# Kernel optimization log

Hardware: AMD Instinct MI355X
Metric: run time of the kernel (lower is better)

The kernel has to match this reference:

```python
import jax, jax.numpy as jnp
import numpy as np

B, N, C, H = 16, 4096, 256, 4
D = C // H

def setup_inputs() -> dict:
    key = jax.random.key(0)
    ks = jax.random.split(key, 8)
    w = 0.01  # small init, mimics xavier_uniform gain=0.1
    x = jax.random.normal(ks[0], (B, N, C), jnp.float32)
    S = jax.random.normal(ks[1], (B, H, D, D), jnp.float32) * 0.1
    Wq = jax.random.normal(ks[2], (C, C), jnp.float32) * w
    Wk = jax.random.normal(ks[3], (C, C), jnp.float32) * w
    Wv = jax.random.normal(ks[4], (C, C), jnp.float32) * w
    Wb = jax.random.normal(ks[5], (H, C), jnp.float32) * w  # beta_proj (zeros in torch init; random for nontrivial math)
    Wo = jax.random.normal(ks[6], (C, C), jnp.float32) * w
    g_rms = jnp.ones((C,), jnp.float32)
    return {"x": x, "S": S, "Wq": Wq, "Wk": Wk, "Wv": Wv, "Wb": Wb, "Wo": Wo, "g_rms": g_rms}

def reference(x, S, Wq, Wk, Wv, Wb, Wo, g_rms):
    b, n, c = x.shape
    h = Wb.shape[0]
    d = c // h
    # projections -> (B,H,N,D)
    q = (x @ Wq.T).reshape(b, n, h, d).transpose(0, 2, 1, 3)
    k = (x @ Wk.T).reshape(b, n, h, d).transpose(0, 2, 1, 3)
    v = (x @ Wv.T).reshape(b, n, h, d).transpose(0, 2, 1, 3)
    # feature map + L2 normalize keys
    k = jax.nn.elu(k) + 1.0
    k = k / (jnp.linalg.norm(k, axis=-1, keepdims=True) + 1e-6)
    # per-head gates (B,H,N,1)
    beta = jax.nn.sigmoid(jnp.einsum('bnc,hc->bhn', x, Wb))[..., None]
    # decay + state read
    Sd = S * 0.95
    y = jnp.einsum('bhij,bhnj->bhni', Sd, q)
    pred = jnp.einsum('bhij,bhnj->bhni', Sd, k)
    # delta-rule write: outer(mean weighted error, mean key)
    w_err = jnp.mean(beta * (v - pred), axis=2)  # (B,H,D)
    w_key = jnp.mean(k, axis=2)                  # (B,H,D)
    S_new = jnp.clip(Sd + jnp.einsum('bhi,bhj->bhij', w_err, w_key), -10.0, 10.0)
    # merge heads, RMSNorm, output projection
    y = y.transpose(0, 2, 1, 3).reshape(b, n, c)
    y = y * jax.lax.rsqrt(jnp.mean(y * y, axis=-1, keepdims=True) + 1e-6) * g_rms
    out = y @ Wo.T
    return out, S_new
```

## Files before the change

### kernel.cpp

```cpp
#include <hip/hip_runtime.h>
#include <math.h>


typedef _Float16 f16;
typedef f16 f16x8 __attribute__((ext_vector_type(8)));
typedef float f32x4 __attribute__((ext_vector_type(4)));

__device__ __forceinline__ f16x8 cvt8(const float* q) {
  float4 a = *(const float4*)q;
  float4 b = *(const float4*)(q + 4);
  f16x8 r;
  r[0] = (f16)a.x; r[1] = (f16)a.y; r[2] = (f16)a.z; r[3] = (f16)a.w;
  r[4] = (f16)b.x; r[5] = (f16)b.y; r[6] = (f16)b.z; r[7] = (f16)b.w;
  return r;
}

__global__ __launch_bounds__(256) void beta_xbsum(
    const float* __restrict__ x, const float* __restrict__ Wb,
    float* __restrict__ betaArr, float* __restrict__ xbsum) {
  const int t = threadIdx.x;
  const int wave = t >> 6, lane = t & 63;
  const int b = blockIdx.x >> 6;
  const int tile = blockIdx.x & 63;
  float4 wb[4];
#pragma unroll
  for (int h = 0; h < 4; ++h) wb[h] = *(const float4*)(Wb + h * 256 + lane * 4);
  float xacc[4][4] = {};
  const size_t rowbase = (size_t)b * 4096 + tile * 64;
  __shared__ float bsh[4][64];
  float4 xv = *(const float4*)(x + (rowbase + wave) * 256 + lane * 4);
#pragma unroll 2
  for (int i = 0; i < 16; ++i) {
    int r = i * 4 + wave;
    float4 nx = xv;
    if (i < 15)
      nx = *(const float4*)(x + (rowbase + r + 4) * 256 + lane * 4);
#pragma unroll
    for (int h = 0; h < 4; ++h) {
      float s = xv.x * wb[h].x + xv.y * wb[h].y + xv.z * wb[h].z + xv.w * wb[h].w;
#pragma unroll
      for (int off = 32; off; off >>= 1) s += __shfl_xor(s, off);
      float bh = 1.f / (1.f + __expf(-s));
      if (lane == h) bsh[h][r] = bh;
      xacc[h][0] += bh * xv.x; xacc[h][1] += bh * xv.y;
      xacc[h][2] += bh * xv.z; xacc[h][3] += bh * xv.w;
    }
    xv = nx;
  }
  __shared__ float xbp[4][4][256];
#pragma unroll
  for (int h = 0; h < 4; ++h)
#pragma unroll
    for (int j = 0; j < 4; ++j) xbp[wave][h][lane * 4 + j] = xacc[h][j];
  __syncthreads();
  {
    int h = t >> 6, r = t & 63;
    betaArr[((size_t)(b * 4 + h) << 12) + tile * 64 + r] = bsh[h][r];
  }
  for (int idx = t; idx < 1024; idx += 256) {
    int h = idx >> 8, c = idx & 255;
    float s = xbp[0][h][c] + xbp[1][h][c] + xbp[2][h][c] + xbp[3][h][c];
    atomicAdd(&xbsum[(b * 4 + h) * 256 + c], s);
  }
}

__global__ __launch_bounds__(256) void kgemm_sums(
    const float* __restrict__ x, const float* __restrict__ Wk,
    const float* __restrict__ betaArr,
    float* __restrict__ ksum, float* __restrict__ kbsum) {
  __shared__ union {
    struct { f16 A[128][72]; f16 B[128][72]; } s;
    f16 K[128][132];
  } u;
  __shared__ float bstage[2][128];
  const int t = threadIdx.x;
  const int m0 = blockIdx.y * 128;
  const int n0 = blockIdx.x * 128;
  const int b = m0 >> 12;
  const int wave = t >> 6, lane = t & 63;
  const int wm = (wave >> 1) * 64, wn = (wave & 1) * 64;
  const int fr = lane & 15, fq = lane >> 4;
  {
    int hh = t >> 7, r = t & 127;
    bstage[hh][r] =
        betaArr[((size_t)(b * 4 + (n0 >> 6) + hh) << 12) + (m0 & 4095) + r];
  }
  f32x4 acc[4][4] = {};
#pragma unroll 1
  for (int kt = 0; kt < 4; ++kt) {
    const int k0 = kt * 64;
#pragma unroll
    for (int i = 0; i < 4; ++i) {
      int id = i * 256 + t;
      int row = id >> 3, cc = id & 7;
      *(f16x8*)&u.s.A[row][cc * 8] =
          cvt8(x + (size_t)(m0 + row) * 256 + k0 + cc * 8);
      *(f16x8*)&u.s.B[row][cc * 8] =
          cvt8(Wk + (size_t)(n0 + row) * 256 + k0 + cc * 8);
    }
    __syncthreads();
#pragma unroll
    for (int ks = 0; ks < 2; ++ks) {
      f16x8 afr[4], bfr[4];
#pragma unroll
      for (int mi = 0; mi < 4; ++mi)
        afr[mi] = *(const f16x8*)&u.s.A[wm + mi * 16 + fr][ks * 32 + fq * 8];
#pragma unroll
      for (int ni = 0; ni < 4; ++ni)
        bfr[ni] = *(const f16x8*)&u.s.B[wn + ni * 16 + fr][ks * 32 + fq * 8];
#pragma unroll
      for (int mi = 0; mi < 4; ++mi)
#pragma unroll
        for (int ni = 0; ni < 4; ++ni)
          acc[mi][ni] = __builtin_amdgcn_mfma_f32_16x16x32_f16(
              afr[mi], bfr[ni], acc[mi][ni], 0, 0, 0);
    }
    __syncthreads();
  }
#pragma unroll
  for (int mi = 0; mi < 4; ++mi)
#pragma unroll
    for (int rr = 0; rr < 4; ++rr) {
      float s = 0.f;
#pragma unroll
      for (int ni = 0; ni < 4; ++ni) {
        float v = acc[mi][ni][rr];
        v = v > 0.f ? v + 1.f : __expf(v);
        acc[mi][ni][rr] = v;
        s += v * v;
      }
#pragma unroll
      for (int off = 1; off < 16; off <<= 1) s += __shfl_xor(s, off);
      float inv = 1.f / (sqrtf(s) + 1e-6f);
#pragma unroll
      for (int ni = 0; ni < 4; ++ni) acc[mi][ni][rr] *= inv;
    }
#pragma unroll
  for (int mi = 0; mi < 4; ++mi)
#pragma unroll
    for (int ni = 0; ni < 4; ++ni)
#pragma unroll
      for (int rr = 0; rr < 4; ++rr)
        u.K[wm + mi * 16 + fq * 4 + rr][wn + ni * 16 + fr] = (f16)acc[mi][ni][rr];
  __syncthreads();
  if (t < 128) {
    const int c = t, hl = c >> 6;
    float sk = 0.f, skb = 0.f;
#pragma unroll 4
    for (int r = 0; r < 128; ++r) {
      float v = (float)u.K[r][c];
      float be = bstage[hl][r];
      sk += v;
      skb += be * v;
    }
    int gh = b * 4 + (n0 >> 6) + hl;
    atomicAdd(&ksum[gh * 64 + (c & 63)], sk);
    atomicAdd(&kbsum[gh * 64 + (c & 63)], skb);
  }
}

__global__ __launch_bounds__(256) void fold_M(
    const float* __restrict__ S, const float* __restrict__ Wq,
    f16* __restrict__ M) {
  const int bh = blockIdx.y;
  const int dq = blockIdx.x;
  const int h = bh & 3;
  const int t = threadIdx.x;
  const float* Sp = S + (size_t)bh * 4096 + dq * 8 * 64;
  const float* Wp = Wq + (size_t)h * 64 * 256 + t;
  float m[8] = {};
#pragma unroll 4
  for (int e = 0; e < 64; ++e) {
    float wv = Wp[e * 256];
#pragma unroll
    for (int dd = 0; dd < 8; ++dd) m[dd] += Sp[dd * 64 + e] * wv;
  }
  f16* Mb = M + (size_t)(bh >> 2) * 65536;
#pragma unroll
  for (int dd = 0; dd < 8; ++dd)
    Mb[(size_t)(h * 64 + dq * 8 + dd) * 256 + t] = (f16)(0.95f * m[dd]);
}

__global__ __launch_bounds__(256) void ygemm_ssq(
    const float* __restrict__ x, int m_base, const f16* __restrict__ M,
    f16* __restrict__ y, float* __restrict__ rowssq) {
  __shared__ f16 As[128][72];
  __shared__ f16 Bs[128][72];
  const int t = threadIdx.x;
  const int m0 = blockIdx.y * 128;
  const int n0 = blockIdx.x * 128;
  const int b = (m_base + m0) >> 12;
  const f16* Mb = M + (size_t)b * 65536;
  const int wave = t >> 6, lane = t & 63;
  const int wm = (wave >> 1) * 64, wn = (wave & 1) * 64;
  const int fr = lane & 15, fq = lane >> 4;
  f32x4 acc[4][4] = {};
#pragma unroll 1
  for (int kt = 0; kt < 4; ++kt) {
    const int k0 = kt * 64;
#pragma unroll
    for (int i = 0; i < 4; ++i) {
      int id = i * 256 + t;
      int row = id >> 3, cc = id & 7;
      *(f16x8*)&As[row][cc * 8] =
          cvt8(x + (size_t)(m_base + m0 + row) * 256 + k0 + cc * 8);
      *(uint4*)&Bs[row][cc * 8] =
          *(const uint4*)(Mb + (size_t)(n0 + row) * 256 + k0 + cc * 8);
    }
    __syncthreads();
#pragma unroll
    for (int ks = 0; ks < 2; ++ks) {
      f16x8 afr[4], bfr[4];
#pragma unroll
      for (int mi = 0; mi < 4; ++mi)
        afr[mi] = *(const f16x8*)&As[wm + mi * 16 + fr][ks * 32 + fq * 8];
#pragma unroll
      for (int ni = 0; ni < 4; ++ni)
        bfr[ni] = *(const f16x8*)&Bs[wn + ni * 16 + fr][ks * 32 + fq * 8];
#pragma unroll
      for (int mi = 0; mi < 4; ++mi)
#pragma unroll
        for (int ni = 0; ni < 4; ++ni)
          acc[mi][ni] = __builtin_amdgcn_mfma_f32_16x16x32_f16(
              afr[mi], bfr[ni], acc[mi][ni], 0, 0, 0);
    }
    __syncthreads();
  }
#pragma unroll
  for (int mi = 0; mi < 4; ++mi)
#pragma unroll
    for (int rr = 0; rr < 4; ++rr) {
      float s = 0.f;
#pragma unroll
      for (int ni = 0; ni < 4; ++ni) {
        float v = acc[mi][ni][rr];
        s += v * v;
        int row = m0 + wm + mi * 16 + fq * 4 + rr;
        int col = n0 + wn + ni * 16 + fr;
        y[(size_t)row * 256 + col] = (f16)v;
      }
#pragma unroll
      for (int off = 1; off < 16; off <<= 1) s += __shfl_xor(s, off);
      if (fr == 0)
        atomicAdd(&rowssq[m0 + wm + mi * 16 + fq * 4 + rr], s);
    }
}

__global__ __launch_bounds__(256) void ogemm_scaled(
    const f16* __restrict__ y, const float* __restrict__ rowssq,
    const float* __restrict__ g_rms, const float* __restrict__ Wo,
    float* __restrict__ out, int m_base) {
  __shared__ f16 As[128][72];
  __shared__ f16 Bs[128][72];
  const int t = threadIdx.x;
  const int m0 = blockIdx.y * 128;
  const int n0 = blockIdx.x * 128;
  const int wave = t >> 6, lane = t & 63;
  const int wm = (wave >> 1) * 64, wn = (wave & 1) * 64;
  const int fr = lane & 15, fq = lane >> 4;
  f32x4 acc[4][4] = {};
#pragma unroll 1
  for (int kt = 0; kt < 4; ++kt) {
    const int k0 = kt * 64;
#pragma unroll
    for (int i = 0; i < 4; ++i) {
      int id = i * 256 + t;
      int row = id >> 3, cc = id & 7;
      float rs = rsqrtf(rowssq[m0 + row] * (1.f / 256.f) + 1e-6f);
      const f16* yp = y + (size_t)(m0 + row) * 256 + k0 + cc * 8;
      const float* gp = g_rms + k0 + cc * 8;
      f16x8 a;
#pragma unroll
      for (int j = 0; j < 8; ++j) a[j] = (f16)((float)yp[j] * rs * gp[j]);
      *(f16x8*)&As[row][cc * 8] = a;
      *(f16x8*)&Bs[row][cc * 8] =
          cvt8(Wo + (size_t)(n0 + row) * 256 + k0 + cc * 8);
    }
    __syncthreads();
#pragma unroll
    for (int ks = 0; ks < 2; ++ks) {
      f16x8 afr[4], bfr[4];
#pragma unroll
      for (int mi = 0; mi < 4; ++mi)
        afr[mi] = *(const f16x8*)&As[wm + mi * 16 + fr][ks * 32 + fq * 8];
#pragma unroll
      for (int ni = 0; ni < 4; ++ni)
        bfr[ni] = *(const f16x8*)&Bs[wn + ni * 16 + fr][ks * 32 + fq * 8];
#pragma unroll
      for (int mi = 0; mi < 4; ++mi)
#pragma unroll
        for (int ni = 0; ni < 4; ++ni)
          acc[mi][ni] = __builtin_amdgcn_mfma_f32_16x16x32_f16(
              afr[mi], bfr[ni], acc[mi][ni], 0, 0, 0);
    }
    __syncthreads();
  }
#pragma unroll
  for (int mi = 0; mi < 4; ++mi)
#pragma unroll
    for (int ni = 0; ni < 4; ++ni)
#pragma unroll
      for (int rr = 0; rr < 4; ++rr) {
        int row = m_base + m0 + wm + mi * 16 + fq * 4 + rr;
        int col = n0 + wn + ni * 16 + fr;
        out[(size_t)row * 256 + col] = acc[mi][ni][rr];
      }
}

__global__ __launch_bounds__(256) void finalize_S(
    const float* __restrict__ S, const float* __restrict__ Wv,
    const float* __restrict__ xbsum, const float* __restrict__ ksum,
    const float* __restrict__ kbsum, float* __restrict__ Sout) {
  const int bh = blockIdx.x;
  const int h = bh & 3;
  const int t = threadIdx.x;
  const int wave = t >> 6, lane = t & 63;
  __shared__ float xb[256], kb[64], key[64], errv[64];
  xb[t] = xbsum[bh * 256 + t];
  if (t < 64) {
    kb[t] = kbsum[bh * 64 + t];
    key[t] = ksum[bh * 64 + t] * (1.f / 4096.f);
  }
  __syncthreads();
#pragma unroll 1
  for (int ri = 0; ri < 16; ++ri) {
    int i = wave * 16 + ri;
    float4 wv4 = *(const float4*)(Wv + (size_t)(h * 64 + i) * 256 + lane * 4);
    float4 xb4 = *(const float4*)(&xb[lane * 4]);
    float s = wv4.x * xb4.x + wv4.y * xb4.y + wv4.z * xb4.z + wv4.w * xb4.w;
    s -= 0.95f * S[(size_t)bh * 4096 + i * 64 + lane] * kb[lane];
#pragma unroll
    for (int off = 32; off; off >>= 1) s += __shfl_xor(s, off);
    if (lane == 0) errv[i] = s * (1.f / 4096.f);
  }
  __syncthreads();
  for (int idx = t; idx < 4096; idx += 256) {
    int i = idx >> 6, j = idx & 63;
    float v = 0.95f * S[(size_t)bh * 4096 + idx] + errv[i] * key[j];
    Sout[(size_t)bh * 4096 + idx] = fminf(10.f, fmaxf(-10.f, v));
  }
}

extern "C" void kernel_launch(void* const* d_in, const int* in_sizes, int n_in,
                              void* d_out, int out_size, void* d_ws, size_t ws_size,
                              hipStream_t stream) {
  const float* x  = (const float*)d_in[0];
  const float* S  = (const float*)d_in[1];
  const float* Wq = (const float*)d_in[2];
  const float* Wk = (const float*)d_in[3];
  const float* Wv = (const float*)d_in[4];
  const float* Wb = (const float*)d_in[5];
  const float* Wo = (const float*)d_in[6];
  const float* g  = (const float*)d_in[7];

  char* w = (char*)d_ws;
  float* betaArr = (float*)w;
  f16*   M       = (f16*)(w + 1048576);
  f16*   y       = (f16*)(w + 3145728);
  float* rowssq  = (float*)(w + 19922944);
  float* xbsum   = (float*)(w + 20185088);
  float* ksum    = (float*)(w + 20250624);
  float* kbsum   = (float*)(w + 20267008);

  float* out  = (float*)d_out;
  float* Sout = out + (size_t)16 * 4096 * 256;

  hipMemsetAsync(w + 19922944, 0, 360448, stream);
  beta_xbsum<<<1024, 256, 0, stream>>>(x, Wb, betaArr, xbsum);
  kgemm_sums<<<dim3(2, 512), 256, 0, stream>>>(x, Wk, betaArr, ksum, kbsum);
  fold_M<<<dim3(8, 64), 256, 0, stream>>>(S, Wq, M);
  for (int half = 0; half < 2; ++half) {
    int m_base = half * 32768;
    ygemm_ssq<<<dim3(2, 256), 256, 0, stream>>>(x, m_base, M, y,
                                                rowssq + half * 32768);
    ogemm_scaled<<<dim3(2, 256), 256, 0, stream>>>(y, rowssq + half * 32768, g,
                                                   Wo, out, m_base);
  }
  finalize_S<<<64, 256, 0, stream>>>(S, Wv, xbsum, ksum, kbsum, Sout);
}
```

Before: 250.7 us.

## Pre-convert x and weights to fp16 once and reuse across GEMM kernels

The beta kernel now also writes an fp16 copy of x, and a new prep kernel converts Wk to fp16 and folds the RMSNorm gain into an fp16 copy of Wo. The k-projection, y and output GEMMs then load fp16 tiles directly instead of re-reading fp32 x and converting it in each kernel. This halves the bytes of x read by the later GEMMs. In exchange it adds an extra 32MB write of xh and needs a larger workspace, with the old path kept as a fallback when the workspace is too small.

```diff
diff --git a/kernel.cpp b/kernel.cpp
--- a/kernel.cpp
+++ b/kernel.cpp
@@ -4,6 +4,7 @@
 
 typedef _Float16 f16;
 typedef f16 f16x8 __attribute__((ext_vector_type(8)));
+typedef f16 f16x4 __attribute__((ext_vector_type(4)));
 typedef float f32x4 __attribute__((ext_vector_type(4)));
 
 __device__ __forceinline__ f16x8 cvt8(const float* q) {
@@ -15,9 +16,23 @@
   return r;
 }
 
-__global__ __launch_bounds__(256) void beta_xbsum(
+__global__ __launch_bounds__(256) void prep_w(
+    const float* __restrict__ Wk, const float* __restrict__ Wo,
+    const float* __restrict__ g, f16* __restrict__ Wkh,
+    f16* __restrict__ Wogh) {
+  int i = blockIdx.x * 256 + threadIdx.x;
+#pragma unroll
+  for (int j = 0; j < 4; ++j) {
+    int idx = i + j * 16384;
+    Wkh[idx] = (f16)Wk[idx];
+    Wogh[idx] = (f16)(Wo[idx] * g[idx & 255]);
+  }
+}
+
+__global__ __launch_bounds__(256) void beta_xbsum_h(
     const float* __restrict__ x, const float* __restrict__ Wb,
-    float* __restrict__ betaArr, float* __restrict__ xbsum) {
+    float* __restrict__ betaArr, float* __restrict__ xbsum,
+    f16* __restrict__ xh) {
   const int t = threadIdx.x;
   const int wave = t >> 6, lane = t & 63;
   const int b = blockIdx.x >> 6;
@@ -35,6 +50,9 @@
     float4 nx = xv;
     if (i < 15)
       nx = *(const float4*)(x + (rowbase + r + 4) * 256 + lane * 4);
+    f16x4 hx;
+    hx[0] = (f16)xv.x; hx[1] = (f16)xv.y; hx[2] = (f16)xv.z; hx[3] = (f16)xv.w;
+    *(f16x4*)(xh + (rowbase + r) * 256 + lane * 4) = hx;
 #pragma unroll
     for (int h = 0; h < 4; ++h) {
       float s = xv.x * wb[h].x + xv.y * wb[h].y + xv.z * wb[h].z + xv.w * wb[h].w;
@@ -64,8 +82,8 @@
   }
 }
 
-__global__ __launch_bounds__(256) void kgemm_sums(
-    const float* __restrict__ x, const float* __restrict__ Wk,
+__global__ __launch_bounds__(256) void kgemm_h(
+    const f16* __restrict__ xh, const f16* __restrict__ Wkh,
     const float* __restrict__ betaArr,
     float* __restrict__ ksum, float* __restrict__ kbsum) {
   __shared__ union {
@@ -93,10 +111,10 @@
     for (int i = 0; i < 4; ++i) {
       int id = i * 256 + t;
       int row = id >> 3, cc = id & 7;
-      *(f16x8*)&u.s.A[row][cc * 8] =
-          cvt8(x + (size_t)(m0 + row) * 256 + k0 + cc * 8);
-      *(f16x8*)&u.s.B[row][cc * 8] =
-          cvt8(Wk + (size_t)(n0 + row) * 256 + k0 + cc * 8);
+      *(uint4*)&u.s.A[row][cc * 8] =
+          *(const uint4*)(xh + (size_t)(m0 + row) * 256 + k0 + cc * 8);
+      *(uint4*)&u.s.B[row][cc * 8] =
+          *(const uint4*)(Wkh + (size_t)(n0 + row) * 256 + k0 + cc * 8);
     }
     __syncthreads();
 #pragma unroll
@@ -181,6 +199,275 @@
     Mb[(size_t)(h * 64 + dq * 8 + dd) * 256 + t] = (f16)(0.95f * m[dd]);
 }
 
+__global__ __launch_bounds__(256) void ygemm_h(
+    const f16* __restrict__ xh, int m_base, const f16* __restrict__ M,
+    f16* __restrict__ y, float* __restrict__ rowssq) {
+  __shared__ f16 As[128][72];
+  __shared__ f16 Bs[128][72];
+  const int t = threadIdx.x;
+  const int m0 = blockIdx.y * 128;
+  const int n0 = blockIdx.x * 128;
+  const int b = (m_base + m0) >> 12;
+  const f16* Mb = M + (size_t)b * 65536;
+  const int wave = t >> 6, lane = t & 63;
+  const int wm = (wave >> 1) * 64, wn = (wave & 1) * 64;
+  const int fr = lane & 15, fq = lane >> 4;
+  f32x4 acc[4][4] = {};
+#pragma unroll 1
+  for (int kt = 0; kt < 4; ++kt) {
+    const int k0 = kt * 64;
+#pragma unroll
+    for (int i = 0; i < 4; ++i) {
+      int id = i * 256 + t;
+      int row = id >> 3, cc = id & 7;
+      *(uint4*)&As[row][cc * 8] =
+          *(const uint4*)(xh + (size_t)(m_base + m0 + row) * 256 + k0 + cc * 8);
+      *(uint4*)&Bs[row][cc * 8] =
+          *(const uint4*)(Mb + (size_t)(n0 + row) * 256 + k0 + cc * 8);
+    }
+    __syncthreads();
+#pragma unroll
+    for (int ks = 0; ks < 2; ++ks) {
+      f16x8 afr[4], bfr[4];
+#pragma unroll
+      for (int mi = 0; mi < 4; ++mi)
+        afr[mi] = *(const f16x8*)&As[wm + mi * 16 + fr][ks * 32 + fq * 8];
+#pragma unroll
+      for (int ni = 0; ni < 4; ++ni)
+        bfr[ni] = *(const f16x8*)&Bs[wn + ni * 16 + fr][ks * 32 + fq * 8];
+#pragma unroll
+      for (int mi = 0; mi < 4; ++mi)
+#pragma unroll
+        for (int ni = 0; ni < 4; ++ni)
+          acc[mi][ni] = __builtin_amdgcn_mfma_f32_16x16x32_f16(
+              afr[mi], bfr[ni], acc[mi][ni], 0, 0, 0);
+    }
+    __syncthreads();
+  }
+#pragma unroll
+  for (int mi = 0; mi < 4; ++mi)
+#pragma unroll
+    for (int rr = 0; rr < 4; ++rr) {
+      float s = 0.f;
+#pragma unroll
+      for (int ni = 0; ni < 4; ++ni) {
+        float v = acc[mi][ni][rr];
+        s += v * v;
+        int row = m0 + wm + mi * 16 + fq * 4 + rr;
+        int col = n0 + wn + ni * 16 + fr;
+        y[(size_t)row * 256 + col] = (f16)v;
+      }
+#pragma unroll
+      for (int off = 1; off < 16; off <<= 1) s += __shfl_xor(s, off);
+      if (fr == 0)
+        atomicAdd(&rowssq[m0 + wm + mi * 16 + fq * 4 + rr], s);
+    }
+}
+
+__global__ __launch_bounds__(256) void ogemm_h(
+    const f16* __restrict__ y, const float* __restrict__ rowssq,
+    const f16* __restrict__ Wogh, float* __restrict__ out, int m_base) {
+  __shared__ f16 As[128][72];
+  __shared__ f16 Bs[128][72];
+  __shared__ float rsl[128];
+  const int t = threadIdx.x;
+  const int m0 = blockIdx.y * 128;
+  const int n0 = blockIdx.x * 128;
+  const int wave = t >> 6, lane = t & 63;
+  const int wm = (wave >> 1) * 64, wn = (wave & 1) * 64;
+  const int fr = lane & 15, fq = lane >> 4;
+  if (t < 128) rsl[t] = rsqrtf(rowssq[m0 + t] * (1.f / 256.f) + 1e-6f);
+  f32x4 acc[4][4] = {};
+#pragma unroll 1
+  for (int kt = 0; kt < 4; ++kt) {
+    const int k0 = kt * 64;
+#pragma unroll
+    for (int i = 0; i < 4; ++i) {
+      int id = i * 256 + t;
+      int row = id >> 3, cc = id & 7;
+      *(uint4*)&As[row][cc * 8] =
+          *(const uint4*)(y + (size_t)(m0 + row) * 256 + k0 + cc * 8);
+      *(uint4*)&Bs[row][cc * 8] =
+          *(const uint4*)(Wogh + (size_t)(n0 + row) * 256 + k0 + cc * 8);
+    }
+    __syncthreads();
+#pragma unroll
+    for (int ks = 0; ks < 2; ++ks) {
+      f16x8 afr[4], bfr[4];
+#pragma unroll
+      for (int mi = 0; mi < 4; ++mi)
+        afr[mi] = *(const f16x8*)&As[wm + mi * 16 + fr][ks * 32 + fq * 8];
+#pragma unroll
+      for (int ni = 0; ni < 4; ++ni)
+        bfr[ni] = *(const f16x8*)&Bs[wn + ni * 16 + fr][ks * 32 + fq * 8];
+#pragma unroll
+      for (int mi = 0; mi < 4; ++mi)
+#pragma unroll
+        for (int ni = 0; ni < 4; ++ni)
+          acc[mi][ni] = __builtin_amdgcn_mfma_f32_16x16x32_f16(
+              afr[mi], bfr[ni], acc[mi][ni], 0, 0, 0);
+    }
+    __syncthreads();
+  }
+#pragma unroll
+  for (int mi = 0; mi < 4; ++mi)
+#pragma unroll
+    for (int rr = 0; rr < 4; ++rr) {
+      int lrow = wm + mi * 16 + fq * 4 + rr;
+      float rs = rsl[lrow];
+#pragma unroll
+      for (int ni = 0; ni < 4; ++ni) {
+        int row = m_base + m0 + lrow;
+        int col = n0 + wn + ni * 16 + fr;
+        out[(size_t)row * 256 + col] = rs * acc[mi][ni][rr];
+      }
+    }
+}
+
+__global__ __launch_bounds__(256) void beta_xbsum(
+    const float* __restrict__ x, const float* __restrict__ Wb,
+    float* __restrict__ betaArr, float* __restrict__ xbsum) {
+  const int t = threadIdx.x;
+  const int wave = t >> 6, lane = t & 63;
+  const int b = blockIdx.x >> 6;
+  const int tile = blockIdx.x & 63;
+  float4 wb[4];
+#pragma unroll
+  for (int h = 0; h < 4; ++h) wb[h] = *(const float4*)(Wb + h * 256 + lane * 4);
+  float xacc[4][4] = {};
+  const size_t rowbase = (size_t)b * 4096 + tile * 64;
+  __shared__ float bsh[4][64];
+  float4 xv = *(const float4*)(x + (rowbase + wave) * 256 + lane * 4);
+#pragma unroll 2
+  for (int i = 0; i < 16; ++i) {
+    int r = i * 4 + wave;
+    float4 nx = xv;
+    if (i < 15)
+      nx = *(const float4*)(x + (rowbase + r + 4) * 256 + lane * 4);
+#pragma unroll
+    for (int h = 0; h < 4; ++h) {
+      float s = xv.x * wb[h].x + xv.y * wb[h].y + xv.z * wb[h].z + xv.w * wb[h].w;
+#pragma unroll
+      for (int off = 32; off; off >>= 1) s += __shfl_xor(s, off);
+      float bh = 1.f / (1.f + __expf(-s));
+      if (lane == h) bsh[h][r] = bh;
+      xacc[h][0] += bh * xv.x; xacc[h][1] += bh * xv.y;
+      xacc[h][2] += bh * xv.z; xacc[h][3] += bh * xv.w;
+    }
+    xv = nx;
+  }
+  __shared__ float xbp[4][4][256];
+#pragma unroll
+  for (int h = 0; h < 4; ++h)
+#pragma unroll
+    for (int j = 0; j < 4; ++j) xbp[wave][h][lane * 4 + j] = xacc[h][j];
+  __syncthreads();
+  {
+    int h = t >> 6, r = t & 63;
+    betaArr[((size_t)(b * 4 + h) << 12) + tile * 64 + r] = bsh[h][r];
+  }
+  for (int idx = t; idx < 1024; idx += 256) {
+    int h = idx >> 8, c = idx & 255;
+    float s = xbp[0][h][c] + xbp[1][h][c] + xbp[2][h][c] + xbp[3][h][c];
+    atomicAdd(&xbsum[(b * 4 + h) * 256 + c], s);
+  }
+}
+
+__global__ __launch_bounds__(256) void kgemm_sums(
+    const float* __restrict__ x, const float* __restrict__ Wk,
+    const float* __restrict__ betaArr,
+    float* __restrict__ ksum, float* __restrict__ kbsum) {
+  __shared__ union {
+    struct { f16 A[128][72]; f16 B[128][72]; } s;
+    f16 K[128][132];
+  } u;
+  __shared__ float bstage[2][128];
+  const int t = threadIdx.x;
+  const int m0 = blockIdx.y * 128;
+  const int n0 = blockIdx.x * 128;
+  const int b = m0 >> 12;
+  const int wave = t >> 6, lane = t & 63;
+  const int wm = (wave >> 1) * 64, wn = (wave & 1) * 64;
+  const int fr = lane & 15, fq = lane >> 4;
+  {
+    int hh = t >> 7, r = t & 127;
+    bstage[hh][r] =
+        betaArr[((size_t)(b * 4 + (n0 >> 6) + hh) << 12) + (m0 & 4095) + r];
+  }
+  f32x4 acc[4][4] = {};
+#pragma unroll 1
+  for (int kt = 0; kt < 4; ++kt) {
+    const int k0 = kt * 64;
+#pragma unroll
+    for (int i = 0; i < 4; ++i) {
+      int id = i * 256 + t;
+      int row = id >> 3, cc = id & 7;
+      *(f16x8*)&u.s.A[row][cc * 8] =
+          cvt8(x + (size_t)(m0 + row) * 256 + k0 + cc * 8);
+      *(f16x8*)&u.s.B[row][cc * 8] =
+          cvt8(Wk + (size_t)(n0 + row) * 256 + k0 + cc * 8);
+    }
+    __syncthreads();
+#pragma unroll
+    for (int ks = 0; ks < 2; ++ks) {
+      f16x8 afr[4], bfr[4];
+#pragma unroll
+      for (int mi = 0; mi < 4; ++mi)
+        afr[mi] = *(const f16x8*)&u.s.A[wm + mi * 16 + fr][ks * 32 + fq * 8];
+#pragma unroll
+      for (int ni = 0; ni < 4; ++ni)
+        bfr[ni] = *(const f16x8*)&u.s.B[wn + ni * 16 + fr][ks * 32 + fq * 8];
+#pragma unroll
+      for (int mi = 0; mi < 4; ++mi)
+#pragma unroll
+        for (int ni = 0; ni < 4; ++ni)
+          acc[mi][ni] = __builtin_amdgcn_mfma_f32_16x16x32_f16(
+              afr[mi], bfr[ni], acc[mi][ni], 0, 0, 0);
+    }
+    __syncthreads();
+  }
+#pragma unroll
+  for (int mi = 0; mi < 4; ++mi)
+#pragma unroll
+    for (int rr = 0; rr < 4; ++rr) {
+      float s = 0.f;
+#pragma unroll
+      for (int ni = 0; ni < 4; ++ni) {
+        float v = acc[mi][ni][rr];
+        v = v > 0.f ? v + 1.f : __expf(v);
+        acc[mi][ni][rr] = v;
+        s += v * v;
+      }
+#pragma unroll
+      for (int off = 1; off < 16; off <<= 1) s += __shfl_xor(s, off);
+      float inv = 1.f / (sqrtf(s) + 1e-6f);
+#pragma unroll
+      for (int ni = 0; ni < 4; ++ni) acc[mi][ni][rr] *= inv;
+    }
+#pragma unroll
+  for (int mi = 0; mi < 4; ++mi)
+#pragma unroll
+    for (int ni = 0; ni < 4; ++ni)
+#pragma unroll
+      for (int rr = 0; rr < 4; ++rr)
+        u.K[wm + mi * 16 + fq * 4 + rr][wn + ni * 16 + fr] = (f16)acc[mi][ni][rr];
+  __syncthreads();
+  if (t < 128) {
+    const int c = t, hl = c >> 6;
+    float sk = 0.f, skb = 0.f;
+#pragma unroll 4
+    for (int r = 0; r < 128; ++r) {
+      float v = (float)u.K[r][c];
+      float be = bstage[hl][r];
+      sk += v;
+      skb += be * v;
+    }
+    int gh = b * 4 + (n0 >> 6) + hl;
+    atomicAdd(&ksum[gh * 64 + (c & 63)], sk);
+    atomicAdd(&kbsum[gh * 64 + (c & 63)], skb);
+  }
+}
+
 __global__ __launch_bounds__(256) void ygemm_ssq(
     const float* __restrict__ x, int m_base, const f16* __restrict__ M,
     f16* __restrict__ y, float* __restrict__ rowssq) {
@@ -361,20 +648,39 @@
   float* xbsum   = (float*)(w + 20185088);
   float* ksum    = (float*)(w + 20250624);
   float* kbsum   = (float*)(w + 20267008);
+  f16*   xh      = (f16*)(w + 20283392);
+  f16*   Wkh     = (f16*)(w + 53837824);
+  f16*   Wogh    = (f16*)(w + 53968896);
+  const size_t WS_NEED = 54099968ull;
 
   float* out  = (float*)d_out;
   float* Sout = out + (size_t)16 * 4096 * 256;
 
   hipMemsetAsync(w + 19922944, 0, 360448, stream);
-  beta_xbsum<<<1024, 256, 0, stream>>>(x, Wb, betaArr, xbsum);
-  kgemm_sums<<<dim3(2, 512), 256, 0, stream>>>(x, Wk, betaArr, ksum, kbsum);
-  fold_M<<<dim3(8, 64), 256, 0, stream>>>(S, Wq, M);
-  for (int half = 0; half < 2; ++half) {
-    int m_base = half * 32768;
-    ygemm_ssq<<<dim3(2, 256), 256, 0, stream>>>(x, m_base, M, y,
+
+  if (ws_size >= WS_NEED) {
+    prep_w<<<64, 256, 0, stream>>>(Wk, Wo, g, Wkh, Wogh);
+    beta_xbsum_h<<<1024, 256, 0, stream>>>(x, Wb, betaArr, xbsum, xh);
+    kgemm_h<<<dim3(2, 512), 256, 0, stream>>>(xh, Wkh, betaArr, ksum, kbsum);
+    fold_M<<<dim3(8, 64), 256, 0, stream>>>(S, Wq, M);
+    for (int half = 0; half < 2; ++half) {
+      int m_base = half * 32768;
+      ygemm_h<<<dim3(2, 256), 256, 0, stream>>>(xh, m_base, M, y,
                                                 rowssq + half * 32768);
-    ogemm_scaled<<<dim3(2, 256), 256, 0, stream>>>(y, rowssq + half * 32768, g,
-                                                   Wo, out, m_base);
+      ogemm_h<<<dim3(2, 256), 256, 0, stream>>>(y, rowssq + half * 32768,
+                                                Wogh, out, m_base);
+    }
+  } else {
+    beta_xbsum<<<1024, 256, 0, stream>>>(x, Wb, betaArr, xbsum);
+    kgemm_sums<<<dim3(2, 512), 256, 0, stream>>>(x, Wk, betaArr, ksum, kbsum);
+    fold_M<<<dim3(8, 64), 256, 0, stream>>>(S, Wq, M);
+    for (int half = 0; half < 2; ++half) {
+      int m_base = half * 32768;
+      ygemm_ssq<<<dim3(2, 256), 256, 0, stream>>>(x, m_base, M, y,
+                                                  rowssq + half * 32768);
+      ogemm_scaled<<<dim3(2, 256), 256, 0, stream>>>(y, rowssq + half * 32768,
+                                                     g, Wo, out, m_base);
+    }
   }
   finalize_S<<<64, 256, 0, stream>>>(S, Wv, xbsum, ksum, kbsum, Sout);
 }
```

Result: faster. 235.8 us (-5.9%).
